# Performance work log

Hardware: AMD Instinct MI355X
Metric: run time of the kernel (lower is better)

## Reference

```python
import jax, jax.numpy as jnp
import numpy as np

# Parallel-beam 2D geometry (PYRO-NN style defaults for a 512^2 volume)
N_ANGLES = 720      # projections over [0, pi)
N_DET = 725         # ~ceil(sqrt(2)*512) detector bins, spacing 1 px
N_SAMP = 768        # samples along each ray, spacing 1 px
DET_SP = 1.0
SAMP_SP = 1.0


def _bilinear(img, xs, ys):
    """Bilinear sample img[H,W] at float coords (xs, ys); zero outside."""
    H, W = img.shape
    x0 = jnp.floor(xs)
    y0 = jnp.floor(ys)
    wx = xs - x0
    wy = ys - y0
    x0i = x0.astype(jnp.int32)
    y0i = y0.astype(jnp.int32)

    def gather(yi, xi):
        valid = (xi >= 0) & (xi < W) & (yi >= 0) & (yi < H)
        v = img[jnp.clip(yi, 0, H - 1), jnp.clip(xi, 0, W - 1)]
        return jnp.where(valid, v, jnp.zeros((), img.dtype))

    v00 = gather(y0i, x0i)
    v01 = gather(y0i, x0i + 1)
    v10 = gather(y0i + 1, x0i)
    v11 = gather(y0i + 1, x0i + 1)
    return (v00 * (1 - wx) + v01 * wx) * (1 - wy) + (v10 * (1 - wx) + v11 * wx) * wy


def _project(img):
    """Parallel-beam forward projection (Radon transform) of img[H,W] -> sino[A,D]."""
    H, W = img.shape
    cx = (W - 1) * 0.5
    cy = (H - 1) * 0.5
    # detector coordinates s and ray-integration coordinates t, centered
    s = (jnp.arange(N_DET, dtype=jnp.float32) - (N_DET - 1) * 0.5) * DET_SP
    t = (jnp.arange(N_SAMP, dtype=jnp.float32) - (N_SAMP - 1) * 0.5) * SAMP_SP
    angles = jnp.linspace(0.0, np.pi, N_ANGLES, endpoint=False, dtype=jnp.float32)

    def per_angle(th):
        c = jnp.cos(th)
        sn = jnp.sin(th)
        # point = s * detector_axis + t * ray_direction   [D, T]
        xs = s[:, None] * c - t[None, :] * sn + cx
        ys = s[:, None] * sn + t[None, :] * c + cy
        # line integral: sum of samples * step size
        return _bilinear(img, xs, ys).sum(axis=1) * SAMP_SP

    # lax.map over angles keeps the [D,T] sampling grid per-angle (memory-friendly)
    return jax.lax.map(per_angle, angles)  # [A, D]


def setup_inputs() -> dict:
    key = jax.random.key(0)
    k1, k2 = jax.random.split(key)
    x = jax.random.normal(k1, (1, 512, 512), dtype=jnp.float32)
    reco = jax.random.normal(k2, (1, 512, 512), dtype=jnp.float32)
    return {"x": x, "reco": reco}


def reference(x, reco):
    updated_reco = x + reco                     # [1, H, W]
    current_sino = jax.vmap(_project)(updated_reco)  # [1, A, D]
    return (current_sino, reco)
```

## Files before the change

kernel.cpp:

```cpp
#include <hip/hip_runtime.h>
#include <hip/hip_fp16.h>
#include <math.h>

#define N_ANGLES 720
#define N_DET    725
#define N_SAMP   768
#define IMG_H    512
#define IMG_W    512

#define QW       520
#define QROWB    2080u
#define QBYTES   ((size_t)QW * QW * 4)

#define A_BLOCKS  (181 * 3)
#define B1_ANG    358
#define B1G       90
#define B1_DT     91
#define B1N       (B1G * B1_DT)
#define B2_ANG    181
#define B2_DBLK   46
#define B2N       (B2_ANG * B2_DBLK)

typedef _Float16 f16x2 __attribute__((ext_vector_type(2)));

struct Q2 { unsigned lo, hi; };

__device__ __forceinline__ f16x2 pkrtz(float a, float b) {
    auto t = __builtin_amdgcn_cvt_pkrtz(a, b);
    union { decltype(t) s; f16x2 d; } u;
    u.s = t;
    return u.d;
}

__device__ __forceinline__ float fdot2f(f16x2 a, f16x2 b, float c) {
    using hraw = decltype(__builtin_amdgcn_cvt_pkrtz(0.0f, 0.0f));
    union { f16x2 s; hraw d; } ua, ub;
    ua.s = a;
    ub.s = b;
    return __builtin_amdgcn_fdot2(ua.d, ub.d, c, false);
}

__device__ __forceinline__ float img_at(const float* __restrict__ x,
                                        const float* __restrict__ r,
                                        int py, int px) {
    if ((unsigned)py < IMG_H && (unsigned)px < IMG_W) {
        int i = py * IMG_W + px;
        return x[i] + r[i];
    }
    return 0.0f;
}

__global__ __launch_bounds__(256) void build_q9(const float* __restrict__ x,
                                                const float* __restrict__ r,
                                                unsigned* __restrict__ Q,
                                                float* __restrict__ out2) {
    int t = blockIdx.x * 256 + threadIdx.x;
    if (t < (IMG_H * IMG_W / 4))
        ((float4*)out2)[t] = ((const float4*)r)[t];
    int cell = t * 8;
    if (cell >= QW * QW) return;
    int jy  = cell / QW;
    int jx0 = cell - jy * QW;
    int fy  = jy - 4;
    unsigned o[8];
    #pragma unroll
    for (int e = 0; e < 8; ++e) {
        float v0 = img_at(x, r, fy,     jx0 - 4 + e);
        float v1 = img_at(x, r, fy + 1, jx0 - 4 + e);
        union { f16x2 h; unsigned u; } p;
        p.h = pkrtz(v0, v1);
        o[e] = p.u;
    }
    *(uint4*)(&Q[cell])     = *(uint4*)(&o[0]);
    *(uint4*)(&Q[cell + 4]) = *(uint4*)(&o[4]);
}

template<int U>
__device__ __forceinline__ float run_ray(const char* __restrict__ Qb,
                                         float xs, float ys,
                                         float dx, float dy, int nb) {
    float acc = 0.0f;
    for (int k = 0; k < nb; ++k) {
        unsigned offs[U];
        float wxs[U], wys[U];
        Q2 qv[U];
        #pragma unroll
        for (int u = 0; u < U; ++u) {
            float xu = fmaf((float)u, dx, xs);
            float yu = fmaf((float)u, dy, ys);
            xu = fminf(fmaxf(xu, 0.0f), 518.0f);
            yu = fminf(fmaxf(yu, 0.0f), 518.0f);
            unsigned jx = (unsigned)xu;
            unsigned jy = (unsigned)yu;
            wxs[u] = __builtin_amdgcn_fractf(xu);
            wys[u] = __builtin_amdgcn_fractf(yu);
            offs[u] = (unsigned)__umul24(jy, QROWB) + (jx << 2);
        }
        #pragma unroll
        for (int u = 0; u < U; ++u)
            qv[u] = *(const Q2*)(Qb + offs[u]);
        #pragma unroll
        for (int u = 0; u < U; ++u) {
            union { unsigned w; f16x2 h; } L, R;
            L.w = qv[u].lo;
            R.w = qv[u].hi;
            f16x2 dlr = R.h - L.h;
            f16x2 tb  = dlr * pkrtz(wxs[u], wxs[u]) + L.h;
            acc = fdot2f(tb, pkrtz(1.0f - wys[u], wys[u]), acc);
        }
        xs = fmaf((float)U, dx, xs);
        ys = fmaf((float)U, dy, ys);
    }
    return acc;
}

__device__ __forceinline__ void clip4(float X0, float Y0, float sn, float c,
                                      int& i0, int& i1) {
    float ilo = 0.0f, ihi = (float)(N_SAMP - 1);
    if (fabsf(sn) > 1e-6f) {
        float rr = -1.0f / sn;
        float a1 = (3.0f   - X0) * rr;
        float a2 = (516.0f - X0) * rr;
        ilo = fmaxf(ilo, fminf(a1, a2));
        ihi = fminf(ihi, fmaxf(a1, a2));
    } else if (X0 <= 3.0f || X0 >= 516.0f) {
        ihi = -1.0f;
    }
    if (fabsf(c) > 1e-6f) {
        float rr = 1.0f / c;
        float a1 = (3.0f   - Y0) * rr;
        float a2 = (516.0f - Y0) * rr;
        ilo = fmaxf(ilo, fminf(a1, a2));
        ihi = fminf(ihi, fmaxf(a1, a2));
    } else if (Y0 <= 3.0f || Y0 >= 516.0f) {
        ihi = -1.0f;
    }
    if (ihi < ilo) { i0 = 1 << 20; i1 = -(1 << 20); return; }
    i0 = max(0, (int)ilo - 1);
    i1 = min(N_SAMP - 1, (int)ihi + 1);
}

__global__ __launch_bounds__(256, 8) void project_fc(const unsigned* __restrict__ Q,
                                                     float* __restrict__ sino) {
    const char* __restrict__ Qb = (const char*)Q;
    const int bid = blockIdx.x;
    const int tid = threadIdx.x;

    if (bid < A_BLOCKS) {
        const int a_idx = bid / 3;
        const int a  = (a_idx <= 90) ? a_idx : a_idx + 539;
        const int dt = (bid % 3) * 256 + tid;
        const int d  = min(dt, N_DET - 1);
        const int lane = tid & 63;

        const float th = (float)((double)a * (M_PI / 720.0));
        const float c  = cosf(th);
        const float sn = sinf(th);
        const float s  = (float)d - 362.0f;
        const float X0 = fmaf(s, c, 259.5f) + 383.5f * sn;
        const float Y0 = fmaf(s, sn, 259.5f) - 383.5f * c;

        const int dsh = -(int)rintf((float)lane * (sn / c));

        int i0, i1;
        clip4(X0, Y0, sn, c, i0, i1);
        int a0 = i0 - dsh, a1 = i1 - dsh;
        #pragma unroll
        for (int m = 1; m <= 32; m <<= 1) {
            a0 = min(a0, __shfl_xor(a0, m, 64));
            a1 = max(a1, __shfl_xor(a1, m, 64));
        }
        const int trips = __builtin_amdgcn_readfirstlane(a1 - a0 + 1);
        const int nb = (trips + 7) >> 3;

        const float I0 = (float)(a0 + dsh);
        float xs = fmaf(I0, -sn, X0);
        float ys = fmaf(I0,  c,  Y0);
        float acc = run_ray<8>(Qb, xs, ys, -sn, c, nb);
        if (dt < N_DET) sino[a * N_DET + dt] = acc;
    } else if (bid < A_BLOCKS + B1N) {
        const int idx   = bid - A_BLOCKS;
        const int g     = idx / B1_DT;
        const int dtile = idx - g * B1_DT;
        const int wv    = tid >> 6;
        int ang = g * 4 + wv;
        if (ang > B1_ANG - 1) ang = B1_ANG - 1;
        const int a     = (ang < 179) ? (91 + ang) : (451 + (ang - 179));
        const int lane  = tid & 63;
        const int dl    = lane & 7;
        const int tl    = lane >> 3;
        const int dt    = dtile * 8 + dl;
        const int d     = min(dt, N_DET - 1);

        const float th = (float)((double)a * (M_PI / 720.0));
        const float c  = cosf(th);
        const float sn = sinf(th);
        const float s  = (float)d - 362.0f;
        const float X0 = fmaf(s, c, 259.5f) + 383.5f * sn;
        const float Y0 = fmaf(s, sn, 259.5f) - 383.5f * c;

        const int dsh = -(int)rintf((float)dl * (sn / c));

        int i0, i1;
        clip4(X0, Y0, sn, c, i0, i1);
        int a0 = i0 - dsh, a1 = i1 - dsh;
        #pragma unroll
        for (int m = 1; m <= 32; m <<= 1) {
            a0 = min(a0, __shfl_xor(a0, m, 64));
            a1 = max(a1, __shfl_xor(a1, m, 64));
        }
        const int span  = __builtin_amdgcn_readfirstlane(a1 - a0 + 1);
        const int trips = (span + 8) >> 3;
        const int nb    = (trips + 3) >> 2;

        const float I0 = (float)(a0 + dsh + tl);
        float xs = fmaf(I0, -sn, X0);
        float ys = fmaf(I0,  c,  Y0);
        float acc = run_ray<4>(Qb, xs, ys, -8.0f * sn, 8.0f * c, nb);

        acc += __shfl_xor(acc, 8, 64);
        acc += __shfl_xor(acc, 16, 64);
        acc += __shfl_xor(acc, 32, 64);
        if (tl == 0 && dt < N_DET) sino[a * N_DET + dt] = acc;
    } else {
        const int idx  = bid - A_BLOCKS - B1N;
        const int a    = 270 + idx / B2_DBLK;
        const int dblk = idx % B2_DBLK;
        const int lane = tid & 63;
        const int tl   = lane & 15;
        const int grp  = lane >> 4;
        const int wv   = tid >> 6;
        const int d    = dblk * 16 + wv * 4 + grp;

        const float th = (float)((double)a * (M_PI / 720.0));
        const float c  = cosf(th);
        const float sn = sinf(th);
        const float s  = (float)d - 362.0f;
        const float X0 = fmaf(s, c, 259.5f) + 383.5f * sn;
        const float Y0 = fmaf(s, sn, 259.5f) - 383.5f * c;

        int i0, i1;
        clip4(X0, Y0, sn, c, i0, i1);
        i0 = min(i0, __shfl_xor(i0, 16, 64));
        i0 = min(i0, __shfl_xor(i0, 32, 64));
        i1 = max(i1, __shfl_xor(i1, 16, 64));
        i1 = max(i1, __shfl_xor(i1, 32, 64));
        const int span  = __builtin_amdgcn_readfirstlane(i1 - i0 + 1);
        const int trips = (span + 15) >> 4;
        const int nb    = (trips + 3) >> 2;

        float xs = fmaf((float)(i0 + tl), -sn, X0);
        float ys = fmaf((float)(i0 + tl),  c,  Y0);
        float acc = run_ray<4>(Qb, xs, ys, -16.0f * sn, 16.0f * c, nb);

        acc += __shfl_xor(acc, 1, 64);
        acc += __shfl_xor(acc, 2, 64);
        acc += __shfl_xor(acc, 4, 64);
        acc += __shfl_xor(acc, 8, 64);
        if (tl == 0 && d < N_DET) sino[a * N_DET + d] = acc;
    }
}

extern "C" void kernel_launch(void* const* d_in, const int* in_sizes, int n_in,
                              void* d_out, int out_size, void* d_ws, size_t ws_size,
                              hipStream_t stream) {
    const float* x    = (const float*)d_in[0];
    const float* reco = (const float*)d_in[1];
    float* out = (float*)d_out;

    if (ws_size >= QBYTES) {
        unsigned* Q = (unsigned*)d_ws;
        const int nthreads = (IMG_H * IMG_W / 4 > QW * QW / 8)
                                 ? IMG_H * IMG_W / 4 : QW * QW / 8;
        build_q9<<<(nthreads + 255) / 256, 256, 0, stream>>>(x, reco, Q,
                                                            out + N_ANGLES * N_DET);
        project_fc<<<A_BLOCKS + B1N + B2N, 256, 0, stream>>>(Q, out);
    }
}
```

Baseline: 165.3 us.

## Store vertical differences in table and use bounds-checked buffer loads

```diff
diff --git a/kernel.cpp b/kernel.cpp
--- a/kernel.cpp
+++ b/kernel.cpp
@@ -22,8 +22,8 @@
 #define B2N       (B2_ANG * B2_DBLK)
 
 typedef _Float16 f16x2 __attribute__((ext_vector_type(2)));
-
-struct Q2 { unsigned lo, hi; };
+typedef unsigned u32x2 __attribute__((ext_vector_type(2)));
+typedef unsigned u32x4 __attribute__((ext_vector_type(4)));
 
 __device__ __forceinline__ f16x2 pkrtz(float a, float b) {
     auto t = __builtin_amdgcn_cvt_pkrtz(a, b);
@@ -40,6 +40,16 @@
     return __builtin_amdgcn_fdot2(ua.d, ub.d, c, false);
 }
 
+__device__ __forceinline__ u32x4 make_rsrc(const void* p, unsigned bytes) {
+    unsigned long long a = (unsigned long long)p;
+    u32x4 r;
+    r.x = (unsigned)a;
+    r.y = (unsigned)(a >> 32) & 0xFFFFu;
+    r.z = bytes;
+    r.w = 0x00020000u;
+    return r;
+}
+
 __device__ __forceinline__ float img_at(const float* __restrict__ x,
                                         const float* __restrict__ r,
                                         int py, int px) {
@@ -50,7 +60,7 @@
     return 0.0f;
 }
 
-__global__ __launch_bounds__(256) void build_q9(const float* __restrict__ x,
+__global__ __launch_bounds__(256) void build_qa(const float* __restrict__ x,
                                                 const float* __restrict__ r,
                                                 unsigned* __restrict__ Q,
                                                 float* __restrict__ out2) {
@@ -68,7 +78,7 @@
         float v0 = img_at(x, r, fy,     jx0 - 4 + e);
         float v1 = img_at(x, r, fy + 1, jx0 - 4 + e);
         union { f16x2 h; unsigned u; } p;
-        p.h = pkrtz(v0, v1);
+        p.h = pkrtz(v0, v1 - v0);
         o[e] = p.u;
     }
     *(uint4*)(&Q[cell])     = *(uint4*)(&o[0]);
@@ -76,37 +86,39 @@
 }
 
 template<int U>
-__device__ __forceinline__ float run_ray(const char* __restrict__ Qb,
+__device__ __forceinline__ float run_ray(u32x4 rsrc,
                                          float xs, float ys,
                                          float dx, float dy, int nb) {
     float acc = 0.0f;
     for (int k = 0; k < nb; ++k) {
         unsigned offs[U];
         float wxs[U], wys[U];
-        Q2 qv[U];
+        u32x2 qv[U];
         #pragma unroll
         for (int u = 0; u < U; ++u) {
             float xu = fmaf((float)u, dx, xs);
             float yu = fmaf((float)u, dy, ys);
             xu = fminf(fmaxf(xu, 0.0f), 518.0f);
-            yu = fminf(fmaxf(yu, 0.0f), 518.0f);
             unsigned jx = (unsigned)xu;
-            unsigned jy = (unsigned)yu;
+            int      jy = (int)yu;
             wxs[u] = __builtin_amdgcn_fractf(xu);
             wys[u] = __builtin_amdgcn_fractf(yu);
-            offs[u] = (unsigned)__umul24(jy, QROWB) + (jx << 2);
+            offs[u] = (unsigned)__umul24((unsigned)jy, QROWB) + (jx << 2);
         }
         #pragma unroll
         for (int u = 0; u < U; ++u)
-            qv[u] = *(const Q2*)(Qb + offs[u]);
+            asm volatile("buffer_load_dwordx2 %0, %1, %2, 0 offen"
+                         : "=v"(qv[u]) : "v"(offs[u]), "s"(rsrc));
+        asm volatile("s_waitcnt vmcnt(0)" ::: "memory");
+        __builtin_amdgcn_sched_barrier(0);
         #pragma unroll
         for (int u = 0; u < U; ++u) {
             union { unsigned w; f16x2 h; } L, R;
-            L.w = qv[u].lo;
-            R.w = qv[u].hi;
+            L.w = qv[u].x;
+            R.w = qv[u].y;
             f16x2 dlr = R.h - L.h;
             f16x2 tb  = dlr * pkrtz(wxs[u], wxs[u]) + L.h;
-            acc = fdot2f(tb, pkrtz(1.0f - wys[u], wys[u]), acc);
+            acc = fdot2f(tb, pkrtz(1.0f, wys[u]), acc);
         }
         xs = fmaf((float)U, dx, xs);
         ys = fmaf((float)U, dy, ys);
@@ -140,9 +152,9 @@
     i1 = min(N_SAMP - 1, (int)ihi + 1);
 }
 
-__global__ __launch_bounds__(256, 8) void project_fc(const unsigned* __restrict__ Q,
+__global__ __launch_bounds__(256, 8) void project_fd(const unsigned* __restrict__ Q,
                                                      float* __restrict__ sino) {
-    const char* __restrict__ Qb = (const char*)Q;
+    const u32x4 rsrc = make_rsrc(Q, (unsigned)QBYTES);
     const int bid = blockIdx.x;
     const int tid = threadIdx.x;
 
@@ -176,7 +188,7 @@
         const float I0 = (float)(a0 + dsh);
         float xs = fmaf(I0, -sn, X0);
         float ys = fmaf(I0,  c,  Y0);
-        float acc = run_ray<8>(Qb, xs, ys, -sn, c, nb);
+        float acc = run_ray<8>(rsrc, xs, ys, -sn, c, nb);
         if (dt < N_DET) sino[a * N_DET + dt] = acc;
     } else if (bid < A_BLOCKS + B1N) {
         const int idx   = bid - A_BLOCKS;
@@ -216,7 +228,7 @@
         const float I0 = (float)(a0 + dsh + tl);
         float xs = fmaf(I0, -sn, X0);
         float ys = fmaf(I0,  c,  Y0);
-        float acc = run_ray<4>(Qb, xs, ys, -8.0f * sn, 8.0f * c, nb);
+        float acc = run_ray<4>(rsrc, xs, ys, -8.0f * sn, 8.0f * c, nb);
 
         acc += __shfl_xor(acc, 8, 64);
         acc += __shfl_xor(acc, 16, 64);
@@ -251,7 +263,7 @@
 
         float xs = fmaf((float)(i0 + tl), -sn, X0);
         float ys = fmaf((float)(i0 + tl),  c,  Y0);
-        float acc = run_ray<4>(Qb, xs, ys, -16.0f * sn, 16.0f * c, nb);
+        float acc = run_ray<4>(rsrc, xs, ys, -16.0f * sn, 16.0f * c, nb);
 
         acc += __shfl_xor(acc, 1, 64);
         acc += __shfl_xor(acc, 2, 64);
@@ -272,8 +284,8 @@
         unsigned* Q = (unsigned*)d_ws;
         const int nthreads = (IMG_H * IMG_W / 4 > QW * QW / 8)
                                  ? IMG_H * IMG_W / 4 : QW * QW / 8;
-        build_q9<<<(nthreads + 255) / 256, 256, 0, stream>>>(x, reco, Q,
+        build_qa<<<(nthreads + 255) / 256, 256, 0, stream>>>(x, reco, Q,
                                                             out + N_ANGLES * N_DET);
-        project_fc<<<A_BLOCKS + B1N + B2N, 256, 0, stream>>>(Q, out);
-    }
-}
+        project_fd<<<A_BLOCKS + B1N + B2N, 256, 0, stream>>>(Q, out);
+    }
+}
```

After: 163.9 us. Within noise of the previous version (-0.9%).
